# Performance work log

Measured on AMD Instinct MI355X. Metric: run time of the kernel, lower is better.

The kernel has to match this reference:

```python
import jax, jax.numpy as jnp
import numpy as np

B, S, DIM = 8, 1, 2048
H = 16
QLR, KVLR = 1536, 512
DN, DR, DV = 128, 64, 128      # qk_nope, qk_rope, v head dims
START = 8191                    # start_pos; end_pos = START + S = 8192
EPS = 1e-6
SCALE = (DN + DR) ** -0.5


def _rms(x, w):
    # F.rms_norm: x / sqrt(mean(x^2)+eps) * w
    return x * w * jax.lax.rsqrt(jnp.mean(jnp.square(x), axis=-1, keepdims=True) + EPS)


def _rope(x, cos, sin):
    # x: [..., r]; consecutive pairs (x0,x1) treated as complex, multiplied by cos+i*sin
    xr, xi = x[..., 0::2], x[..., 1::2]
    out_r = xr * cos - xi * sin
    out_i = xr * sin + xi * cos
    return jnp.stack([out_r, out_i], axis=-1).reshape(x.shape)


def setup_inputs() -> dict:
    key = jax.random.key(0)
    ks = jax.random.split(key, 12)
    # rotary tables for the single decode position
    inv_freq = 1.0 / (10000.0 ** (np.arange(0, DR, 2, dtype=np.float32) / DR))  # [DR/2]
    pos = np.arange(START, START + S, dtype=np.float32)[:, None]                # [S,1]
    ang = pos * inv_freq[None, :]                                               # [S, DR/2]
    return {
        "x": jax.random.normal(ks[0], (B, S, DIM), jnp.float32),
        "start_pos": START,
        "freqs_cos": jnp.asarray(np.cos(ang)),
        "freqs_sin": jnp.asarray(np.sin(ang)),
        "kv_cache_prefix": jax.random.normal(ks[1], (B, START, KVLR), jnp.float32),
        "pe_cache_prefix": jax.random.normal(ks[2], (B, START, DR), jnp.float32),
        "wq_a_w": jax.random.normal(ks[3], (QLR, DIM), jnp.float32) * 0.02,
        "wq_a_b": jnp.zeros((QLR,), jnp.float32),
        "q_norm_w": jnp.ones((QLR,), jnp.float32),
        "wq_b_w": jax.random.normal(ks[4], (H * (DN + DR), QLR), jnp.float32) * 0.02,
        "wq_b_b": jnp.zeros((H * (DN + DR),), jnp.float32),
        "wkv_a_w": jax.random.normal(ks[5], (KVLR + DR, DIM), jnp.float32) * 0.02,
        "wkv_a_b": jnp.zeros((KVLR + DR,), jnp.float32),
        "kv_norm_w": jnp.ones((KVLR,), jnp.float32),
        "wkv_b_w": jax.random.normal(ks[6], (H * (DN + DV), KVLR), jnp.float32) * 0.02,
        "wo_w": jax.random.normal(ks[7], (DIM, H * DV), jnp.float32) * 0.02,
        "wo_b": jnp.zeros((DIM,), jnp.float32),
    }


def reference(x, start_pos, freqs_cos, freqs_sin, kv_cache_prefix, pe_cache_prefix,
              wq_a_w, wq_a_b, q_norm_w, wq_b_w, wq_b_b,
              wkv_a_w, wkv_a_b, kv_norm_w, wkv_b_w, wo_w, wo_b):
    b, s, _ = x.shape
    # low-rank query projection
    q = _rms(x @ wq_a_w.T + wq_a_b, q_norm_w) @ wq_b_w.T + wq_b_b
    q = q.reshape(b, s, H, DN + DR)
    q_nope, q_pe = q[..., :DN], q[..., DN:]
    cos = freqs_cos[None, :, None, :]  # [1,s,1,DR/2]
    sin = freqs_sin[None, :, None, :]
    q_pe = _rope(q_pe, cos, sin)
    # compressed KV + rope key branch
    kvpe = x @ wkv_a_w.T + wkv_a_b               # [b,s,KVLR+DR]
    kv, k_pe = kvpe[..., :KVLR], kvpe[..., KVLR:]
    k_pe = _rope(k_pe[:, :, None, :], cos, sin)[:, :, 0, :]
    # weight absorption: project q_nope into latent space through wkv_b's K-part
    wkv_b = wkv_b_w.reshape(H, DN + DV, KVLR)
    q_abs = jnp.einsum('bshd,hdc->bshc', q_nope, wkv_b[:, :DN])
    # append current step to caches
    kv_cache = jnp.concatenate([kv_cache_prefix, _rms(kv, kv_norm_w)], axis=1)  # [b,t,KVLR]
    pe_cache = jnp.concatenate([pe_cache_prefix, k_pe], axis=1)                 # [b,t,DR]
    # attention in latent space (seqlen=1 decode -> no causal mask needed)
    scores = (jnp.einsum('bshc,btc->bsht', q_abs, kv_cache)
              + jnp.einsum('bshr,btr->bsht', q_pe, pe_cache)) * SCALE
    attn = jax.nn.softmax(scores.astype(jnp.float32), axis=-1).astype(x.dtype)
    out = jnp.einsum('bsht,btc->bshc', attn, kv_cache)
    out = jnp.einsum('bshc,hdc->bshd', out, wkv_b[:, DN:])  # V-part of wkv_b
    return out.reshape(b, s, H * DV) @ wo_w.T + wo_b
```

## Files before the change

### kernel.cpp

```cpp
#include <hip/hip_runtime.h>
#include <math.h>

namespace {
constexpr int B_   = 8;
constexpr int DIM_ = 2048;
constexpr int H_   = 16;
constexpr int QLR_ = 1536;
constexpr int KVLR_= 512;
constexpr int DN_  = 128;
constexpr int DR_  = 64;
constexpr int DV_  = 128;
constexpr int TPRE_= 8191;
constexpr int CE_  = 576;
constexpr int NCH_ = 32;
constexpr int CT_  = 256;
constexpr float EPS_ = 1e-6f;
constexpr float SCALE_ = 0.07216878364870322f;
constexpr int SSTR_ = 20;

constexpr size_t WS_QLAT  = 0;
constexpr size_t WS_KVPE  = WS_QLAT  + (size_t)B_*QLR_;
constexpr size_t WS_KVNEW = WS_KVPE  + (size_t)B_*CE_;
constexpr size_t WS_PENEW = WS_KVNEW + (size_t)B_*KVLR_;
constexpr size_t WS_QRS   = WS_PENEW + (size_t)B_*DR_;
constexpr size_t WS_QNOPE = WS_QRS   + (size_t)B_;
constexpr size_t WS_QT    = WS_QNOPE + (size_t)B_*H_*DN_;
constexpr size_t WS_MLOC  = WS_QT    + (size_t)B_*CE_*H_;
constexpr size_t WS_LLOC  = WS_MLOC  + (size_t)B_*H_*NCH_;
constexpr size_t WS_OUT2  = WS_LLOC  + (size_t)B_*H_*NCH_;
constexpr size_t WS_OPART = WS_OUT2  + (size_t)B_*DIM_;
}

__global__ __launch_bounds__(256) void mla_k1(const float* __restrict__ x,
                                              const float* __restrict__ wqa,
                                              const float* __restrict__ bqa,
                                              const float* __restrict__ wkva,
                                              const float* __restrict__ bkva,
                                              float* __restrict__ ws) {
  const int w = threadIdx.x >> 6, l = threadIdx.x & 63;
  const int r = blockIdx.x * 4 + w;
  const float* W; const float* bias; float* out; int rr; int ostride;
  if (r < QLR_) { W = wqa;  bias = bqa;  out = ws + WS_QLAT; rr = r;        ostride = QLR_; }
  else          { W = wkva; bias = bkva; out = ws + WS_KVPE; rr = r - QLR_; ostride = CE_;  }
  const float4* wp = (const float4*)(W + (size_t)rr * DIM_);
  const float4* x4 = (const float4*)x;
  float4 wv[8];
#pragma unroll
  for (int j = 0; j < 8; ++j) wv[j] = wp[l + 64 * j];
  float acc[B_];
#pragma unroll
  for (int b = 0; b < B_; ++b) acc[b] = 0.f;
#pragma unroll
  for (int b = 0; b < B_; ++b) {
#pragma unroll
    for (int j = 0; j < 8; ++j) {
      const float4 xv = x4[b * (DIM_ / 4) + l + 64 * j];
      acc[b] = fmaf(wv[j].x, xv.x, fmaf(wv[j].y, xv.y, fmaf(wv[j].z, xv.z, fmaf(wv[j].w, xv.w, acc[b]))));
    }
  }
#pragma unroll
  for (int b = 0; b < B_; ++b)
#pragma unroll
    for (int s = 32; s; s >>= 1) acc[b] += __shfl_xor(acc[b], s);
  if (l == 0) {
    const float b0 = bias[rr];
#pragma unroll
    for (int b = 0; b < B_; ++b) out[b * ostride + rr] = acc[b] + b0;
  }
}

__global__ __launch_bounds__(256) void mla_k2(const float* __restrict__ kvnw,
                                              const float* __restrict__ fcos,
                                              const float* __restrict__ fsin,
                                              float* __restrict__ ws) {
  const int tid = threadIdx.x;
  const int b = tid >> 5, i = tid & 31;
  const float* kvpe = ws + WS_KVPE + b * CE_;
  float ss = 0.f;
#pragma unroll
  for (int j = 0; j < KVLR_ / 32; ++j) { const float v = kvpe[i + 32 * j]; ss = fmaf(v, v, ss); }
#pragma unroll
  for (int s = 16; s; s >>= 1) ss += __shfl_xor(ss, s, 32);
  const float scale = 1.0f / sqrtf(ss / (float)KVLR_ + EPS_);
  float* kvn = ws + WS_KVNEW + b * KVLR_;
#pragma unroll
  for (int j = 0; j < KVLR_ / 32; ++j) {
    const int c = i + 32 * j;
    kvn[c] = kvpe[c] * kvnw[c] * scale;
  }
  {
    const float xr = kvpe[KVLR_ + 2 * i], xi = kvpe[KVLR_ + 2 * i + 1];
    const float c = fcos[i], s = fsin[i];
    float* pen = ws + WS_PENEW + b * DR_;
    pen[2 * i]     = xr * c - xi * s;
    pen[2 * i + 1] = xr * s + xi * c;
  }
  {
    const float* p = ws + WS_QLAT + b * QLR_;
    float sq = 0.f;
#pragma unroll
    for (int j = 0; j < QLR_ / 32; ++j) { const float v = p[i + 32 * j]; sq = fmaf(v, v, sq); }
#pragma unroll
    for (int s = 16; s; s >>= 1) sq += __shfl_xor(sq, s, 32);
    if (i == 0) ws[WS_QRS + b] = 1.0f / sqrtf(sq / (float)QLR_ + EPS_);
  }
}

__global__ __launch_bounds__(256) void mla_k3(const float* __restrict__ qnw,
                                              const float* __restrict__ wqb,
                                              const float* __restrict__ bqb,
                                              const float* __restrict__ fcos,
                                              const float* __restrict__ fsin,
                                              float* __restrict__ ws) {
  const int w = threadIdx.x >> 6, l = threadIdx.x & 63;
  const int r0 = blockIdx.x * 8 + w * 2;
  const float4* w0p = (const float4*)(wqb + (size_t)r0 * QLR_);
  const float4* w1p = (const float4*)(wqb + (size_t)(r0 + 1) * QLR_);
  const float4* g4  = (const float4*)qnw;
  const float4* x4  = (const float4*)(ws + WS_QLAT);
  float4 wg0[6], wg1[6];
#pragma unroll
  for (int j = 0; j < 6; ++j) {
    const int c4 = l + 64 * j;
    const float4 a = w0p[c4], bb = w1p[c4], g = g4[c4];
    wg0[j].x = a.x * g.x; wg0[j].y = a.y * g.y; wg0[j].z = a.z * g.z; wg0[j].w = a.w * g.w;
    wg1[j].x = bb.x * g.x; wg1[j].y = bb.y * g.y; wg1[j].z = bb.z * g.z; wg1[j].w = bb.w * g.w;
  }
  float acc0[B_], acc1[B_];
#pragma unroll
  for (int b = 0; b < B_; ++b) { acc0[b] = 0.f; acc1[b] = 0.f; }
#pragma unroll
  for (int b = 0; b < B_; ++b) {
#pragma unroll
    for (int j = 0; j < 6; ++j) {
      const float4 xv = x4[b * (QLR_ / 4) + l + 64 * j];
      acc0[b] = fmaf(wg0[j].x, xv.x, fmaf(wg0[j].y, xv.y, fmaf(wg0[j].z, xv.z, fmaf(wg0[j].w, xv.w, acc0[b]))));
      acc1[b] = fmaf(wg1[j].x, xv.x, fmaf(wg1[j].y, xv.y, fmaf(wg1[j].z, xv.z, fmaf(wg1[j].w, xv.w, acc1[b]))));
    }
  }
#pragma unroll
  for (int b = 0; b < B_; ++b)
#pragma unroll
    for (int s = 32; s; s >>= 1) {
      acc0[b] += __shfl_xor(acc0[b], s);
      acc1[b] += __shfl_xor(acc1[b], s);
    }
  if (l == 0) {
    const int h = r0 / (DN_ + DR_);
    const int j0 = r0 - h * (DN_ + DR_);
    const float b0 = bqb[r0], b1 = bqb[r0 + 1];
    if (j0 < DN_) {
      float* qn = ws + WS_QNOPE;
#pragma unroll
      for (int b = 0; b < B_; ++b) {
        const float sb = ws[WS_QRS + b];
        qn[(b * H_ + h) * DN_ + j0]     = acc0[b] * sb + b0;
        qn[(b * H_ + h) * DN_ + j0 + 1] = acc1[b] * sb + b1;
      }
    } else {
      const int i = (j0 - DN_) >> 1;
      const float c = fcos[i], s = fsin[i];
      float* qT = ws + WS_QT;
#pragma unroll
      for (int b = 0; b < B_; ++b) {
        const float sb = ws[WS_QRS + b];
        const float xr = acc0[b] * sb + b0, xi = acc1[b] * sb + b1;
        qT[((size_t)b * CE_ + KVLR_ + 2 * i) * H_ + h]     = xr * c - xi * s;
        qT[((size_t)b * CE_ + KVLR_ + 2 * i + 1) * H_ + h] = xr * s + xi * c;
      }
    }
  }
}

__global__ __launch_bounds__(256) void mla_k4(const float* __restrict__ wkvb,
                                              float* __restrict__ ws) {
  __shared__ float red[7 * 32 * B_];
  const int h = blockIdx.y;
  const int strip = blockIdx.x;
  const int tid = threadIdx.x;
  const int c = tid & 31, dg = tid >> 5;
  const int cg = strip * 32 + c;
  const float* qn = ws + WS_QNOPE;
  float acc[B_];
#pragma unroll
  for (int b = 0; b < B_; ++b) acc[b] = 0.f;
  const float* wp = wkvb + (size_t)h * 256 * KVLR_ + cg;
#pragma unroll
  for (int dd = 0; dd < 16; ++dd) {
    const int d = dg * 16 + dd;
    const float wv = wp[(size_t)d * KVLR_];
#pragma unroll
    for (int b = 0; b < B_; ++b) acc[b] = fmaf(qn[(b * H_ + h) * DN_ + d], wv, acc[b]);
  }
  if (dg > 0) {
#pragma unroll
    for (int b = 0; b < B_; ++b) red[(((dg - 1) * 32) + c) * B_ + b] = acc[b];
  }
  __syncthreads();
  if (dg == 0) {
    float* qT = ws + WS_QT;
#pragma unroll
    for (int b = 0; b < B_; ++b) {
      float v = acc[b];
#pragma unroll
      for (int g = 0; g < 7; ++g) v += red[(g * 32 + c) * B_ + b];
      qT[((size_t)b * CE_ + cg) * H_ + h] = v;
    }
  }
}

__global__ __launch_bounds__(256) void mla_k5(const float* __restrict__ kvpre,
                                              const float* __restrict__ pepre,
                                              float* __restrict__ ws) {
  __shared__ float sl[CT_ * SSTR_];
  const int b = blockIdx.y;
  const int chunk = blockIdx.x;
  const int t0 = chunk * CT_;
  const int tid = threadIdx.x;
  const int w = tid >> 6, l = tid & 63;
  const float* kvnew = ws + WS_KVNEW;
  const float* penew = ws + WS_PENEW;

  {
    const int t = t0 + (w << 6) + l;
    const float* kvrow; const float* perow;
    if (t < TPRE_) {
      kvrow = kvpre + ((size_t)b * TPRE_ + t) * KVLR_;
      perow = pepre + ((size_t)b * TPRE_ + t) * DR_;
    } else {
      kvrow = kvnew + b * KVLR_;
      perow = penew + b * DR_;
    }
    const float* qTb = ws + WS_QT + (size_t)b * CE_ * H_;
    float acc[H_];
#pragma unroll
    for (int h = 0; h < H_; ++h) acc[h] = 0.f;
    auto fma4 = [&](const float4 k, const float* qc) {
#pragma unroll
      for (int h = 0; h < H_; ++h) {
        acc[h] = fmaf(qc[h],          k.x, acc[h]);
        acc[h] = fmaf(qc[H_ + h],     k.y, acc[h]);
        acc[h] = fmaf(qc[2 * H_ + h], k.z, acc[h]);
        acc[h] = fmaf(qc[3 * H_ + h], k.w, acc[h]);
      }
    };
    for (int c16 = 0; c16 < KVLR_; c16 += 16) {
      const float4 k0 = *(const float4*)(kvrow + c16);
      const float4 k1 = *(const float4*)(kvrow + c16 + 4);
      const float4 k2 = *(const float4*)(kvrow + c16 + 8);
      const float4 k3 = *(const float4*)(kvrow + c16 + 12);
      const float* qc = qTb + (size_t)c16 * H_;
      fma4(k0, qc);
      fma4(k1, qc + 4 * H_);
      fma4(k2, qc + 8 * H_);
      fma4(k3, qc + 12 * H_);
    }
    {
      const float4 k0 = *(const float4*)(perow);
      const float4 k1 = *(const float4*)(perow + 4);
      const float4 k2 = *(const float4*)(perow + 8);
      const float4 k3 = *(const float4*)(perow + 12);
      const float4 k4 = *(const float4*)(perow + 16);
      const float4 k5 = *(const float4*)(perow + 20);
      const float4 k6 = *(const float4*)(perow + 24);
      const float4 k7 = *(const float4*)(perow + 28);
      const float* qc = qTb + (size_t)KVLR_ * H_;
      fma4(k0, qc);            fma4(k1, qc + 4 * H_);
      fma4(k2, qc + 8 * H_);   fma4(k3, qc + 12 * H_);
      fma4(k4, qc + 16 * H_);  fma4(k5, qc + 20 * H_);
      fma4(k6, qc + 24 * H_);  fma4(k7, qc + 28 * H_);
      const float4 k8 = *(const float4*)(perow + 32);
      const float4 k9 = *(const float4*)(perow + 36);
      const float4 ka = *(const float4*)(perow + 40);
      const float4 kb = *(const float4*)(perow + 44);
      const float4 kc = *(const float4*)(perow + 48);
      const float4 kd = *(const float4*)(perow + 52);
      const float4 ke = *(const float4*)(perow + 56);
      const float4 kf = *(const float4*)(perow + 60);
      fma4(k8, qc + 32 * H_);  fma4(k9, qc + 36 * H_);
      fma4(ka, qc + 40 * H_);  fma4(kb, qc + 44 * H_);
      fma4(kc, qc + 48 * H_);  fma4(kd, qc + 52 * H_);
      fma4(ke, qc + 56 * H_);  fma4(kf, qc + 60 * H_);
    }
    const int tl = (w << 6) + l;
#pragma unroll
    for (int g = 0; g < 4; ++g) {
      float4 v;
      v.x = acc[4 * g] * SCALE_; v.y = acc[4 * g + 1] * SCALE_;
      v.z = acc[4 * g + 2] * SCALE_; v.w = acc[4 * g + 3] * SCALE_;
      *(float4*)(sl + tl * SSTR_ + 4 * g) = v;
    }
  }
  __syncthreads();

  {
    const int h2 = tid >> 4, grp = tid & 15;
    float m = -3.4e38f;
#pragma unroll
    for (int j = 0; j < 16; ++j) m = fmaxf(m, sl[(grp + 16 * j) * SSTR_ + h2]);
#pragma unroll
    for (int s = 8; s; s >>= 1) m = fmaxf(m, __shfl_xor(m, s, 16));
    float lsum = 0.f;
#pragma unroll
    for (int j = 0; j < 16; ++j) {
      const int idx = (grp + 16 * j) * SSTR_ + h2;
      const float p = __expf(sl[idx] - m);
      sl[idx] = p;
      lsum += p;
    }
#pragma unroll
    for (int s = 8; s; s >>= 1) lsum += __shfl_xor(lsum, s, 16);
    if (grp == 0) {
      ws[WS_MLOC + (b * H_ + h2) * NCH_ + chunk] = m;
      ws[WS_LLOC + (b * H_ + h2) * NCH_ + chunk] = lsum;
    }
  }
  __syncthreads();

  {
    float o[4][8];
#pragma unroll
    for (int a = 0; a < 4; ++a)
#pragma unroll
      for (int j = 0; j < 8; ++j) o[a][j] = 0.f;
    const int hb = w * 4;
    const float* kvb = kvpre + (size_t)b * TPRE_ * KVLR_;
    auto step = [&](const float* kr, int t) {
      const float4 p = *(const float4*)(sl + t * SSTR_ + hb);
#pragma unroll
      for (int j = 0; j < 4; ++j) {
        const float2 kv = *(const float2*)(kr + j * 128 + 2 * l);
        o[0][2 * j]     = fmaf(p.x, kv.x, o[0][2 * j]);
        o[0][2 * j + 1] = fmaf(p.x, kv.y, o[0][2 * j + 1]);
        o[1][2 * j]     = fmaf(p.y, kv.x, o[1][2 * j]);
        o[1][2 * j + 1] = fmaf(p.y, kv.y, o[1][2 * j + 1]);
        o[2][2 * j]     = fmaf(p.z, kv.x, o[2][2 * j]);
        o[2][2 * j + 1] = fmaf(p.z, kv.y, o[2][2 * j + 1]);
        o[3][2 * j]     = fmaf(p.w, kv.x, o[3][2 * j]);
        o[3][2 * j + 1] = fmaf(p.w, kv.y, o[3][2 * j + 1]);
      }
    };
    if (t0 + CT_ <= TPRE_) {
#pragma unroll 4
      for (int t = 0; t < CT_; ++t) step(kvb + (size_t)(t0 + t) * KVLR_, t);
    } else {
      const float* kvn = kvnew + b * KVLR_;
      for (int t = 0; t < CT_; ++t) {
        const float* kr = (t0 + t < TPRE_) ? (kvb + (size_t)(t0 + t) * KVLR_) : kvn;
        step(kr, t);
      }
    }
    float* Op = ws + WS_OPART;
#pragma unroll
    for (int a = 0; a < 4; ++a) {
#pragma unroll
      for (int j = 0; j < 4; ++j) {
        float2 v; v.x = o[a][2 * j]; v.y = o[a][2 * j + 1];
        *(float2*)(Op + (((size_t)(b * H_ + hb + a) * NCH_ + chunk) * KVLR_) + j * 128 + 2 * l) = v;
      }
    }
  }
}

__global__ __launch_bounds__(256) void mla_k6(const float* __restrict__ wkvb,
                                              float* __restrict__ ws) {
  const int h = blockIdx.x, b = blockIdx.y;
  __shared__ float wgt[NCH_];
  __shared__ float ao[KVLR_];
  __shared__ float Linv;
  const int tid = threadIdx.x;
  if (tid < NCH_) {
    const float m = ws[WS_MLOC + (b * H_ + h) * NCH_ + tid];
    float M = m;
#pragma unroll
    for (int s = 16; s; s >>= 1) M = fmaxf(M, __shfl_xor(M, s, 32));
    const float wv = __expf(m - M);
    wgt[tid] = wv;
    float lv = ws[WS_LLOC + (b * H_ + h) * NCH_ + tid] * wv;
#pragma unroll
    for (int s = 16; s; s >>= 1) lv += __shfl_xor(lv, s, 32);
    if (tid == 0) Linv = 1.0f / lv;
  }
  __syncthreads();
  const float* Ob = ws + WS_OPART + (size_t)(b * H_ + h) * NCH_ * KVLR_;
  float s0 = 0.f, s1 = 0.f;
#pragma unroll 4
  for (int i = 0; i < NCH_; ++i) {
    const float wv = wgt[i];
    s0 = fmaf(wv, Ob[(size_t)i * KVLR_ + tid], s0);
    s1 = fmaf(wv, Ob[(size_t)i * KVLR_ + tid + 256], s1);
  }
  const float li = Linv;
  ao[tid] = s0 * li;
  ao[tid + 256] = s1 * li;
  __syncthreads();
  const int v = tid >> 1, half = tid & 1;
  const float* w2 = wkvb + ((size_t)h * 256 + DN_ + v) * KVLR_ + half * 256;
  const float* a = ao + half * 256;
  float s = 0.f;
#pragma unroll
  for (int c = 0; c < 256; c += 4) {
    const float4 wv = *(const float4*)(w2 + c);
    s = fmaf(wv.x, a[c], s);
    s = fmaf(wv.y, a[c + 1], s);
    s = fmaf(wv.z, a[c + 2], s);
    s = fmaf(wv.w, a[c + 3], s);
  }
  s += __shfl_xor(s, 1);
  if (half == 0) ws[WS_OUT2 + b * DIM_ + h * DV_ + v] = s;
}

__global__ __launch_bounds__(256) void mla_k7(const float* __restrict__ wo,
                                              const float* __restrict__ wob,
                                              const float* __restrict__ ws,
                                              float* __restrict__ out) {
  const int w = threadIdx.x >> 6, l = threadIdx.x & 63;
  const int r = blockIdx.x * 4 + w;
  const float4* wp = (const float4*)(wo + (size_t)r * DIM_);
  const float4* x4 = (const float4*)(ws + WS_OUT2);
  float4 wv[8];
#pragma unroll
  for (int j = 0; j < 8; ++j) wv[j] = wp[l + 64 * j];
  float acc[B_];
#pragma unroll
  for (int b = 0; b < B_; ++b) acc[b] = 0.f;
#pragma unroll
  for (int b = 0; b < B_; ++b) {
#pragma unroll
    for (int j = 0; j < 8; ++j) {
      const float4 xv = x4[b * (DIM_ / 4) + l + 64 * j];
      acc[b] = fmaf(wv[j].x, xv.x, fmaf(wv[j].y, xv.y, fmaf(wv[j].z, xv.z, fmaf(wv[j].w, xv.w, acc[b]))));
    }
  }
#pragma unroll
  for (int b = 0; b < B_; ++b)
#pragma unroll
    for (int s = 32; s; s >>= 1) acc[b] += __shfl_xor(acc[b], s);
  if (l == 0) {
    const float b0 = wob[r];
#pragma unroll
    for (int b = 0; b < B_; ++b) out[b * DIM_ + r] = acc[b] + b0;
  }
}

extern "C" void kernel_launch(void* const* d_in, const int* in_sizes, int n_in,
                              void* d_out, int out_size, void* d_ws, size_t ws_size,
                              hipStream_t stream) {
  (void)in_sizes; (void)n_in; (void)out_size; (void)ws_size;
  const float* x     = (const float*)d_in[0];
  const float* fcos  = (const float*)d_in[2];
  const float* fsin  = (const float*)d_in[3];
  const float* kvpre = (const float*)d_in[4];
  const float* pepre = (const float*)d_in[5];
  const float* wqa   = (const float*)d_in[6];
  const float* bqa   = (const float*)d_in[7];
  const float* qnw   = (const float*)d_in[8];
  const float* wqb   = (const float*)d_in[9];
  const float* bqb   = (const float*)d_in[10];
  const float* wkva  = (const float*)d_in[11];
  const float* bkva  = (const float*)d_in[12];
  const float* kvnw  = (const float*)d_in[13];
  const float* wkvb  = (const float*)d_in[14];
  const float* wo    = (const float*)d_in[15];
  const float* wob   = (const float*)d_in[16];
  float* ws  = (float*)d_ws;
  float* out = (float*)d_out;

  mla_k1<<<dim3((QLR_ + CE_) / 4), dim3(256), 0, stream>>>(x, wqa, bqa, wkva, bkva, ws);
  mla_k2<<<dim3(1), dim3(256), 0, stream>>>(kvnw, fcos, fsin, ws);
  mla_k3<<<dim3(H_ * (DN_ + DR_) / 8), dim3(256), 0, stream>>>(qnw, wqb, bqb, fcos, fsin, ws);
  mla_k4<<<dim3(16, H_), dim3(256), 0, stream>>>(wkvb, ws);
  mla_k5<<<dim3(NCH_, B_), dim3(256), 0, stream>>>(kvpre, pepre, ws);
  mla_k6<<<dim3(H_, B_), dim3(256), 0, stream>>>(wkvb, ws);
  mla_k7<<<dim3(DIM_ / 4), dim3(256), 0, stream>>>(wo, wob, ws, out);
}
```

Baseline: 411.1 us.

## Restructure attention kernel into flash-style tiled pipeline with shared-memory KV staging

Rewrites the latent attention kernel so that each block streams 8-token tiles of the KV and PE caches through double-buffered shared memory, using register prefetch, and runs an online softmax with running max and sum per head. The KV cache is now read from global memory once per tile and reused for both the score and the output accumulation, where before each element was read twice. The q layout changes to head-major so each thread keeps its slice of q in registers. Chunk count is doubled and chunk size halved to raise parallelism, with the combine kernel updated to match. The cost is more barriers per tile and larger partial-output traffic for the final combine.

```diff
diff --git a/kernel.cpp b/kernel.cpp
--- a/kernel.cpp
+++ b/kernel.cpp
@@ -12,11 +12,13 @@
 constexpr int DV_  = 128;
 constexpr int TPRE_= 8191;
 constexpr int CE_  = 576;
-constexpr int NCH_ = 32;
-constexpr int CT_  = 256;
+constexpr int NCH_ = 64;
+constexpr int CT_  = 128;
+constexpr int TT_  = 8;
+constexpr int NTILE_ = CT_ / TT_;
+constexpr int RSTR_ = 584;
 constexpr float EPS_ = 1e-6f;
 constexpr float SCALE_ = 0.07216878364870322f;
-constexpr int SSTR_ = 20;
 
 constexpr size_t WS_QLAT  = 0;
 constexpr size_t WS_KVPE  = WS_QLAT  + (size_t)B_*QLR_;
@@ -25,7 +27,7 @@
 constexpr size_t WS_QRS   = WS_PENEW + (size_t)B_*DR_;
 constexpr size_t WS_QNOPE = WS_QRS   + (size_t)B_;
 constexpr size_t WS_QT    = WS_QNOPE + (size_t)B_*H_*DN_;
-constexpr size_t WS_MLOC  = WS_QT    + (size_t)B_*CE_*H_;
+constexpr size_t WS_MLOC  = WS_QT    + (size_t)B_*H_*CE_;
 constexpr size_t WS_LLOC  = WS_MLOC  + (size_t)B_*H_*NCH_;
 constexpr size_t WS_OUT2  = WS_LLOC  + (size_t)B_*H_*NCH_;
 constexpr size_t WS_OPART = WS_OUT2  + (size_t)B_*DIM_;
@@ -165,8 +167,8 @@
       for (int b = 0; b < B_; ++b) {
         const float sb = ws[WS_QRS + b];
         const float xr = acc0[b] * sb + b0, xi = acc1[b] * sb + b1;
-        qT[((size_t)b * CE_ + KVLR_ + 2 * i) * H_ + h]     = xr * c - xi * s;
-        qT[((size_t)b * CE_ + KVLR_ + 2 * i + 1) * H_ + h] = xr * s + xi * c;
+        qT[((size_t)b * H_ + h) * CE_ + KVLR_ + 2 * i]     = xr * c - xi * s;
+        qT[((size_t)b * H_ + h) * CE_ + KVLR_ + 2 * i + 1] = xr * s + xi * c;
       }
     }
   }
@@ -204,161 +206,162 @@
       float v = acc[b];
 #pragma unroll
       for (int g = 0; g < 7; ++g) v += red[(g * 32 + c) * B_ + b];
-      qT[((size_t)b * CE_ + cg) * H_ + h] = v;
-    }
-  }
-}
-
-__global__ __launch_bounds__(256) void mla_k5(const float* __restrict__ kvpre,
-                                              const float* __restrict__ pepre,
-                                              float* __restrict__ ws) {
-  __shared__ float sl[CT_ * SSTR_];
-  const int b = blockIdx.y;
-  const int chunk = blockIdx.x;
+      qT[((size_t)b * H_ + h) * CE_ + cg] = v;
+    }
+  }
+}
+
+__global__ __launch_bounds__(256, 3) void mla_k5(const float* __restrict__ kvpre,
+                                                 const float* __restrict__ pepre,
+                                                 float* __restrict__ ws) {
+  __shared__ float buf[2][TT_ * RSTR_];
+  __shared__ float sc[TT_ * 20];
+  __shared__ __align__(16) float mrun[H_], lrun[H_], alf[H_];
+  const int b = blockIdx.y, chunk = blockIdx.x;
   const int t0 = chunk * CT_;
   const int tid = threadIdx.x;
-  const int w = tid >> 6, l = tid & 63;
-  const float* kvnew = ws + WS_KVNEW;
-  const float* penew = ws + WS_PENEW;
-
+  const int l = tid & 63, w = tid >> 6;
+  const int h_s = tid >> 4, sl = tid & 15;
+  const int chalf = w & 1, hh = w >> 1;
+  const float* kvnewb = ws + WS_KVNEW + b * KVLR_;
+  const float* penewb = ws + WS_PENEW + b * DR_;
+
+  if (tid < H_) { mrun[tid] = -3.4e38f; lrun[tid] = 0.f; }
+
+  float4 qreg[9];
   {
-    const int t = t0 + (w << 6) + l;
-    const float* kvrow; const float* perow;
-    if (t < TPRE_) {
-      kvrow = kvpre + ((size_t)b * TPRE_ + t) * KVLR_;
-      perow = pepre + ((size_t)b * TPRE_ + t) * DR_;
-    } else {
-      kvrow = kvnew + b * KVLR_;
-      perow = penew + b * DR_;
-    }
-    const float* qTb = ws + WS_QT + (size_t)b * CE_ * H_;
-    float acc[H_];
-#pragma unroll
-    for (int h = 0; h < H_; ++h) acc[h] = 0.f;
-    auto fma4 = [&](const float4 k, const float* qc) {
-#pragma unroll
-      for (int h = 0; h < H_; ++h) {
-        acc[h] = fmaf(qc[h],          k.x, acc[h]);
-        acc[h] = fmaf(qc[H_ + h],     k.y, acc[h]);
-        acc[h] = fmaf(qc[2 * H_ + h], k.z, acc[h]);
-        acc[h] = fmaf(qc[3 * H_ + h], k.w, acc[h]);
+    const float* qp = ws + WS_QT + ((size_t)b * H_ + h_s) * CE_ + sl * 36;
+#pragma unroll
+    for (int i = 0; i < 9; ++i) qreg[i] = *(const float4*)(qp + 4 * i);
+  }
+  float4 o[8];
+#pragma unroll
+  for (int a = 0; a < 8; ++a) { o[a].x = 0.f; o[a].y = 0.f; o[a].z = 0.f; o[a].w = 0.f; }
+
+  float4 kvr[4]; float4 per;
+  auto issue = [&](int tbase) {
+#pragma unroll
+    for (int k = 0; k < 4; ++k) {
+      const int idx = tid + 256 * k;
+      const int row = idx >> 7, c4 = idx & 127;
+      const int tg = tbase + row;
+      const float* src = (tg < TPRE_) ? (kvpre + ((size_t)b * TPRE_ + tg) * KVLR_ + c4 * 4)
+                                      : (kvnewb + c4 * 4);
+      kvr[k] = *(const float4*)src;
+    }
+    if (tid < 128) {
+      const int row = tid >> 4, c4 = tid & 15;
+      const int tg = tbase + row;
+      const float* src = (tg < TPRE_) ? (pepre + ((size_t)b * TPRE_ + tg) * DR_ + c4 * 4)
+                                      : (penewb + c4 * 4);
+      per = *(const float4*)src;
+    }
+  };
+  auto commit = [&](float* dst) {
+#pragma unroll
+    for (int k = 0; k < 4; ++k) {
+      const int idx = tid + 256 * k;
+      const int row = idx >> 7, c4 = idx & 127;
+      *(float4*)(dst + row * RSTR_ + c4 * 4) = kvr[k];
+    }
+    if (tid < 128) {
+      const int row = tid >> 4, c4 = tid & 15;
+      *(float4*)(dst + row * RSTR_ + 512 + c4 * 4) = per;
+    }
+  };
+
+  issue(t0);
+  commit(buf[0]);
+  __syncthreads();
+
+  for (int j = 0; j < NTILE_; ++j) {
+    const int cur = j & 1;
+    if (j < NTILE_ - 1) issue(t0 + (j + 1) * TT_);
+    const float* bp = buf[cur];
+#pragma unroll
+    for (int tt = 0; tt < TT_; ++tt) {
+      const float* kp = bp + tt * RSTR_ + sl * 36;
+      float4 s4; s4.x = 0.f; s4.y = 0.f; s4.z = 0.f; s4.w = 0.f;
+#pragma unroll
+      for (int i = 0; i < 9; ++i) {
+        const float4 kv = *(const float4*)(kp + 4 * i);
+        s4.x = fmaf(kv.x, qreg[i].x, s4.x);
+        s4.y = fmaf(kv.y, qreg[i].y, s4.y);
+        s4.z = fmaf(kv.z, qreg[i].z, s4.z);
+        s4.w = fmaf(kv.w, qreg[i].w, s4.w);
       }
-    };
-    for (int c16 = 0; c16 < KVLR_; c16 += 16) {
-      const float4 k0 = *(const float4*)(kvrow + c16);
-      const float4 k1 = *(const float4*)(kvrow + c16 + 4);
-      const float4 k2 = *(const float4*)(kvrow + c16 + 8);
-      const float4 k3 = *(const float4*)(kvrow + c16 + 12);
-      const float* qc = qTb + (size_t)c16 * H_;
-      fma4(k0, qc);
-      fma4(k1, qc + 4 * H_);
-      fma4(k2, qc + 8 * H_);
-      fma4(k3, qc + 12 * H_);
-    }
+      float s = (s4.x + s4.y) + (s4.z + s4.w);
+      s += __shfl_xor(s, 1); s += __shfl_xor(s, 2);
+      s += __shfl_xor(s, 4); s += __shfl_xor(s, 8);
+      if (sl == 0) sc[tt * 20 + h_s] = s * SCALE_;
+    }
+    __syncthreads();
+    if (tid < 128) {
+      const int hm = tid >> 3, tm = tid & 7;
+      const float s = sc[tm * 20 + hm];
+      float mt = s;
+      mt = fmaxf(mt, __shfl_xor(mt, 1));
+      mt = fmaxf(mt, __shfl_xor(mt, 2));
+      mt = fmaxf(mt, __shfl_xor(mt, 4));
+      const float mprev = mrun[hm];
+      const float mnew = fmaxf(mprev, mt);
+      const float p = __expf(s - mnew);
+      sc[tm * 20 + hm] = p;
+      float ls = p;
+      ls += __shfl_xor(ls, 1); ls += __shfl_xor(ls, 2); ls += __shfl_xor(ls, 4);
+      if (tm == 0) {
+        const float a = __expf(mprev - mnew);
+        alf[hm] = a;
+        lrun[hm] = lrun[hm] * a + ls;
+        mrun[hm] = mnew;
+      }
+    }
+    __syncthreads();
     {
-      const float4 k0 = *(const float4*)(perow);
-      const float4 k1 = *(const float4*)(perow + 4);
-      const float4 k2 = *(const float4*)(perow + 8);
-      const float4 k3 = *(const float4*)(perow + 12);
-      const float4 k4 = *(const float4*)(perow + 16);
-      const float4 k5 = *(const float4*)(perow + 20);
-      const float4 k6 = *(const float4*)(perow + 24);
-      const float4 k7 = *(const float4*)(perow + 28);
-      const float* qc = qTb + (size_t)KVLR_ * H_;
-      fma4(k0, qc);            fma4(k1, qc + 4 * H_);
-      fma4(k2, qc + 8 * H_);   fma4(k3, qc + 12 * H_);
-      fma4(k4, qc + 16 * H_);  fma4(k5, qc + 20 * H_);
-      fma4(k6, qc + 24 * H_);  fma4(k7, qc + 28 * H_);
-      const float4 k8 = *(const float4*)(perow + 32);
-      const float4 k9 = *(const float4*)(perow + 36);
-      const float4 ka = *(const float4*)(perow + 40);
-      const float4 kb = *(const float4*)(perow + 44);
-      const float4 kc = *(const float4*)(perow + 48);
-      const float4 kd = *(const float4*)(perow + 52);
-      const float4 ke = *(const float4*)(perow + 56);
-      const float4 kf = *(const float4*)(perow + 60);
-      fma4(k8, qc + 32 * H_);  fma4(k9, qc + 36 * H_);
-      fma4(ka, qc + 40 * H_);  fma4(kb, qc + 44 * H_);
-      fma4(kc, qc + 48 * H_);  fma4(kd, qc + 52 * H_);
-      fma4(ke, qc + 56 * H_);  fma4(kf, qc + 60 * H_);
-    }
-    const int tl = (w << 6) + l;
-#pragma unroll
-    for (int g = 0; g < 4; ++g) {
-      float4 v;
-      v.x = acc[4 * g] * SCALE_; v.y = acc[4 * g + 1] * SCALE_;
-      v.z = acc[4 * g + 2] * SCALE_; v.w = acc[4 * g + 3] * SCALE_;
-      *(float4*)(sl + tl * SSTR_ + 4 * g) = v;
-    }
-  }
-  __syncthreads();
-
-  {
-    const int h2 = tid >> 4, grp = tid & 15;
-    float m = -3.4e38f;
-#pragma unroll
-    for (int j = 0; j < 16; ++j) m = fmaxf(m, sl[(grp + 16 * j) * SSTR_ + h2]);
-#pragma unroll
-    for (int s = 8; s; s >>= 1) m = fmaxf(m, __shfl_xor(m, s, 16));
-    float lsum = 0.f;
-#pragma unroll
-    for (int j = 0; j < 16; ++j) {
-      const int idx = (grp + 16 * j) * SSTR_ + h2;
-      const float p = __expf(sl[idx] - m);
-      sl[idx] = p;
-      lsum += p;
-    }
-#pragma unroll
-    for (int s = 8; s; s >>= 1) lsum += __shfl_xor(lsum, s, 16);
-    if (grp == 0) {
-      ws[WS_MLOC + (b * H_ + h2) * NCH_ + chunk] = m;
-      ws[WS_LLOC + (b * H_ + h2) * NCH_ + chunk] = lsum;
-    }
-  }
-  __syncthreads();
-
-  {
-    float o[4][8];
-#pragma unroll
-    for (int a = 0; a < 4; ++a)
-#pragma unroll
-      for (int j = 0; j < 8; ++j) o[a][j] = 0.f;
-    const int hb = w * 4;
-    const float* kvb = kvpre + (size_t)b * TPRE_ * KVLR_;
-    auto step = [&](const float* kr, int t) {
-      const float4 p = *(const float4*)(sl + t * SSTR_ + hb);
-#pragma unroll
-      for (int j = 0; j < 4; ++j) {
-        const float2 kv = *(const float2*)(kr + j * 128 + 2 * l);
-        o[0][2 * j]     = fmaf(p.x, kv.x, o[0][2 * j]);
-        o[0][2 * j + 1] = fmaf(p.x, kv.y, o[0][2 * j + 1]);
-        o[1][2 * j]     = fmaf(p.y, kv.x, o[1][2 * j]);
-        o[1][2 * j + 1] = fmaf(p.y, kv.y, o[1][2 * j + 1]);
-        o[2][2 * j]     = fmaf(p.z, kv.x, o[2][2 * j]);
-        o[2][2 * j + 1] = fmaf(p.z, kv.y, o[2][2 * j + 1]);
-        o[3][2 * j]     = fmaf(p.w, kv.x, o[3][2 * j]);
-        o[3][2 * j + 1] = fmaf(p.w, kv.y, o[3][2 * j + 1]);
+      const float4 a0 = *(const float4*)(alf + hh * 8);
+      const float4 a1 = *(const float4*)(alf + hh * 8 + 4);
+      o[0].x *= a0.x; o[0].y *= a0.x; o[0].z *= a0.x; o[0].w *= a0.x;
+      o[1].x *= a0.y; o[1].y *= a0.y; o[1].z *= a0.y; o[1].w *= a0.y;
+      o[2].x *= a0.z; o[2].y *= a0.z; o[2].z *= a0.z; o[2].w *= a0.z;
+      o[3].x *= a0.w; o[3].y *= a0.w; o[3].z *= a0.w; o[3].w *= a0.w;
+      o[4].x *= a1.x; o[4].y *= a1.x; o[4].z *= a1.x; o[4].w *= a1.x;
+      o[5].x *= a1.y; o[5].y *= a1.y; o[5].z *= a1.y; o[5].w *= a1.y;
+      o[6].x *= a1.z; o[6].y *= a1.z; o[6].z *= a1.z; o[6].w *= a1.z;
+      o[7].x *= a1.w; o[7].y *= a1.w; o[7].z *= a1.w; o[7].w *= a1.w;
+#pragma unroll
+      for (int tt = 0; tt < TT_; ++tt) {
+        const float4 kv = *(const float4*)(bp + tt * RSTR_ + chalf * 256 + 4 * l);
+        const float4 p0 = *(const float4*)(sc + tt * 20 + hh * 8);
+        const float4 p1 = *(const float4*)(sc + tt * 20 + hh * 8 + 4);
+        o[0].x = fmaf(p0.x, kv.x, o[0].x); o[0].y = fmaf(p0.x, kv.y, o[0].y);
+        o[0].z = fmaf(p0.x, kv.z, o[0].z); o[0].w = fmaf(p0.x, kv.w, o[0].w);
+        o[1].x = fmaf(p0.y, kv.x, o[1].x); o[1].y = fmaf(p0.y, kv.y, o[1].y);
+        o[1].z = fmaf(p0.y, kv.z, o[1].z); o[1].w = fmaf(p0.y, kv.w, o[1].w);
+        o[2].x = fmaf(p0.z, kv.x, o[2].x); o[2].y = fmaf(p0.z, kv.y, o[2].y);
+        o[2].z = fmaf(p0.z, kv.z, o[2].z); o[2].w = fmaf(p0.z, kv.w, o[2].w);
+        o[3].x = fmaf(p0.w, kv.x, o[3].x); o[3].y = fmaf(p0.w, kv.y, o[3].y);
+        o[3].z = fmaf(p0.w, kv.z, o[3].z); o[3].w = fmaf(p0.w, kv.w, o[3].w);
+        o[4].x = fmaf(p1.x, kv.x, o[4].x); o[4].y = fmaf(p1.x, kv.y, o[4].y);
+        o[4].z = fmaf(p1.x, kv.z, o[4].z); o[4].w = fmaf(p1.x, kv.w, o[4].w);
+        o[5].x = fmaf(p1.y, kv.x, o[5].x); o[5].y = fmaf(p1.y, kv.y, o[5].y);
+        o[5].z = fmaf(p1.y, kv.z, o[5].z); o[5].w = fmaf(p1.y, kv.w, o[5].w);
+        o[6].x = fmaf(p1.z, kv.x, o[6].x); o[6].y = fmaf(p1.z, kv.y, o[6].y);
+        o[6].z = fmaf(p1.z, kv.z, o[6].z); o[6].w = fmaf(p1.z, kv.w, o[6].w);
+        o[7].x = fmaf(p1.w, kv.x, o[7].x); o[7].y = fmaf(p1.w, kv.y, o[7].y);
+        o[7].z = fmaf(p1.w, kv.z, o[7].z); o[7].w = fmaf(p1.w, kv.w, o[7].w);
       }
-    };
-    if (t0 + CT_ <= TPRE_) {
-#pragma unroll 4
-      for (int t = 0; t < CT_; ++t) step(kvb + (size_t)(t0 + t) * KVLR_, t);
-    } else {
-      const float* kvn = kvnew + b * KVLR_;
-      for (int t = 0; t < CT_; ++t) {
-        const float* kr = (t0 + t < TPRE_) ? (kvb + (size_t)(t0 + t) * KVLR_) : kvn;
-        step(kr, t);
-      }
-    }
-    float* Op = ws + WS_OPART;
-#pragma unroll
-    for (int a = 0; a < 4; ++a) {
-#pragma unroll
-      for (int j = 0; j < 4; ++j) {
-        float2 v; v.x = o[a][2 * j]; v.y = o[a][2 * j + 1];
-        *(float2*)(Op + (((size_t)(b * H_ + hb + a) * NCH_ + chunk) * KVLR_) + j * 128 + 2 * l) = v;
-      }
-    }
+    }
+    if (j < NTILE_ - 1) commit(buf[1 - cur]);
+    __syncthreads();
+  }
+#pragma unroll
+  for (int a = 0; a < 8; ++a) {
+    const int h = hh * 8 + a;
+    *(float4*)(ws + WS_OPART + (((size_t)(b * H_ + h) * NCH_ + chunk) * KVLR_) + chalf * 256 + 4 * l) = o[a];
+  }
+  if (tid < H_) {
+    ws[WS_MLOC + (b * H_ + tid) * NCH_ + chunk] = mrun[tid];
+    ws[WS_LLOC + (b * H_ + tid) * NCH_ + chunk] = lrun[tid];
   }
 }
 
@@ -373,12 +376,12 @@
     const float m = ws[WS_MLOC + (b * H_ + h) * NCH_ + tid];
     float M = m;
 #pragma unroll
-    for (int s = 16; s; s >>= 1) M = fmaxf(M, __shfl_xor(M, s, 32));
+    for (int s = 32; s; s >>= 1) M = fmaxf(M, __shfl_xor(M, s));
     const float wv = __expf(m - M);
     wgt[tid] = wv;
     float lv = ws[WS_LLOC + (b * H_ + h) * NCH_ + tid] * wv;
 #pragma unroll
-    for (int s = 16; s; s >>= 1) lv += __shfl_xor(lv, s, 32);
+    for (int s = 32; s; s >>= 1) lv += __shfl_xor(lv, s);
     if (tid == 0) Linv = 1.0f / lv;
   }
   __syncthreads();
```

After: 591.1 us. 1.44x slower.
